# Kernel optimization log

Measured on AMD Instinct MI355X. Metric: run time of the kernel, lower is better.

## Reference

```python
import jax, jax.numpy as jnp
import numpy as np

DIM = 256
HEADS = 8
GROUPS = 4
HIDDEN = int(DIM * 4.0)
GW = DIM // GROUPS          # group width = 64
HEAD_DIM = DIM // HEADS     # 32
SCALE = HEAD_DIM ** (-0.5)
LN_EPS = 1e-6
BN_EPS = 1e-3               # keras BatchNormalization default epsilon
L2_EPS = 1e-12              # tf.nn.l2_normalize default


def _l2norm(t):
    ss = jnp.sum(t * t, axis=-1, keepdims=True)
    return t * jax.lax.rsqrt(jnp.maximum(ss, L2_EPS))


def setup_inputs() -> dict:
    key = jax.random.key(0)
    ks = jax.random.split(key, 12)
    B, H, W = 16, 56, 56
    x = jax.random.normal(ks[0], (B, H, W, DIM), jnp.float32)
    # depthwise 3x3 kernels for groups 1..GROUPS-1 (group 0's conv is unused in the
    # original code: y0 is a plain slice). Combined depthwise kernel over the last
    # (GROUPS-1)*GW channels, keras HWIO layout with in_ch_per_group = 1.
    dw_kernel = jax.random.normal(ks[1], (3, 3, 1, (GROUPS - 1) * GW), jnp.float32) * 0.05
    dw_bias = jnp.zeros(((GROUPS - 1) * GW,), jnp.float32)
    ln_gamma = jnp.ones((DIM,), jnp.float32)
    ln_beta = jnp.zeros((DIM,), jnp.float32)
    qkv_w = jax.random.normal(ks[2], (DIM, 3 * DIM), jnp.float32) * 0.02  # qkv_bias=False
    proj_w = jax.random.normal(ks[3], (DIM, DIM), jnp.float32) * 0.02
    proj_b = jnp.zeros((DIM,), jnp.float32)
    bn_gamma = jnp.ones((DIM,), jnp.float32)
    bn_beta = jnp.zeros((DIM,), jnp.float32)
    bn_mean = jax.random.normal(ks[4], (DIM,), jnp.float32) * 0.1
    bn_var = jax.random.uniform(ks[5], (DIM,), jnp.float32, 0.5, 1.5)
    fc1_w = jax.random.normal(ks[6], (DIM, HIDDEN), jnp.float32) * 0.02
    fc1_b = jnp.zeros((HIDDEN,), jnp.float32)
    fc2_w = jax.random.normal(ks[7], (HIDDEN, DIM), jnp.float32) * 0.02
    fc2_b = jnp.zeros((DIM,), jnp.float32)
    return dict(x=x, dw_kernel=dw_kernel, dw_bias=dw_bias, ln_gamma=ln_gamma,
                ln_beta=ln_beta, qkv_w=qkv_w, proj_w=proj_w, proj_b=proj_b,
                bn_gamma=bn_gamma, bn_beta=bn_beta, bn_mean=bn_mean, bn_var=bn_var,
                fc1_w=fc1_w, fc1_b=fc1_b, fc2_w=fc2_w, fc2_b=fc2_b)


def _gdta_forward(x, dw_kernel, dw_bias, ln_gamma, ln_beta, qkv_w, proj_w, proj_b,
                  bn_gamma, bn_beta, bn_mean, bn_var, fc1_w, fc1_b, fc2_w, fc2_b):
    B, H, W, C = x.shape
    N = H * W
    # ---- GOTA_block_part1: grouped depthwise convs with cumulative residual ----
    # y0 = x[..., :GW]; for i>=1: K_i = dwconv_i(x_i); y1=K1, y_i = K_i + y_{i-1}
    # => y_i (i>=1) is the cumulative sum of K_1..K_i along the group axis.
    xc = x[..., GW:]  # [B,H,W,(G-1)*GW]
    K = jax.lax.conv_general_dilated(
        xc, dw_kernel, window_strides=(1, 1), padding='SAME',
        dimension_numbers=('NHWC', 'HWIO', 'NHWC'),
        feature_group_count=(GROUPS - 1) * GW) + dw_bias
    Kg = K.reshape(B, H, W, GROUPS - 1, GW)
    Yg = jnp.cumsum(Kg, axis=3).reshape(B, H, W, (GROUPS - 1) * GW)
    dwconv = jnp.concatenate([x[..., :GW], Yg], axis=-1)  # [B,H,W,C]
    # ---- LayerNorm (last axis) ----
    mu = jnp.mean(dwconv, axis=-1, keepdims=True)
    var = jnp.mean(jnp.square(dwconv - mu), axis=-1, keepdims=True)
    norm1 = (dwconv - mu) * jax.lax.rsqrt(var + LN_EPS) * ln_gamma + ln_beta
    t = norm1.reshape(B, N, C)
    # ---- channel (cross-covariance) attention ----
    qkv = (t @ qkv_w).reshape(B, N, 3, HEADS, HEAD_DIM)
    qkv = jnp.transpose(qkv, (2, 0, 3, 1, 4))  # [3,B,h,N,d]
    q, k, v = qkv[0], qkv[1], qkv[2]
    q = _l2norm(q) * SCALE
    k = _l2norm(k)
    attn = jnp.einsum('bhnd,bhne->bhde', q, k)       # [B,h,d,d]
    attn = jax.nn.softmax(attn, axis=-1)
    out = jnp.einsum('bhnd,bhde->bhne', v, attn)     # [B,h,N,d]
    out = jnp.transpose(out, (0, 2, 1, 3)).reshape(B, N, C)
    out = out @ proj_w + proj_b
    attn_img = out.reshape(B, H, W, C)
    # ---- merge + BatchNorm (inference) + MLP + residual ----
    merged = attn_img + dwconv
    merged = (merged - bn_mean) * jax.lax.rsqrt(bn_var + BN_EPS) * bn_gamma + bn_beta
    h1 = jax.nn.gelu(merged @ fc1_w + fc1_b, approximate=False)
    mlp = h1 @ fc2_w + fc2_b
    return x + mlp


def reference(x, dw_kernel, dw_bias, ln_gamma, ln_beta, qkv_w, proj_w, proj_b,
              bn_gamma, bn_beta, bn_mean, bn_var, fc1_w, fc1_b, fc2_w, fc2_b):
    return _gdta_forward(x, dw_kernel, dw_bias, ln_gamma, ln_beta, qkv_w, proj_w,
                         proj_b, bn_gamma, bn_beta, bn_mean, bn_var,
                         fc1_w, fc1_b, fc2_w, fc2_b)
```

## Files before the change

kernel.cpp:

```cpp
#include <hip/hip_runtime.h>
#include <cstdint>

typedef unsigned short u16;
typedef __attribute__((ext_vector_type(8))) _Float16 f16x8;
typedef __attribute__((ext_vector_type(8))) unsigned short u16x8;
typedef __attribute__((ext_vector_type(4))) float f32x4;

#define SPLITN 7

__device__ __forceinline__ float b2f(u16 u) {
  union { unsigned int i; float f; } v; v.i = ((unsigned int)u) << 16; return v.f;
}
__device__ __forceinline__ u16 f2b(float f) {
  union { float f; unsigned int i; } v; v.f = f;
  unsigned int x = v.i;
  return (u16)((x + 0x7fffu + ((x >> 16) & 1u)) >> 16);
}
__device__ __forceinline__ u16 f2h(float f) {
  union { _Float16 h; u16 u; } v; v.h = (_Float16)f; return v.u;
}
__device__ __forceinline__ float h2f(u16 u) {
  union { u16 u; _Float16 h; } v; v.u = u; return (float)v.h;
}
__device__ __forceinline__ float ld(const void* p, long i, int f) {
  return f ? ((const float*)p)[i] : b2f(((const u16*)p)[i]);
}
template<int F>
__device__ __forceinline__ float4 ld4(const void* p, long i) {
  if (F) return *(const float4*)((const float*)p + i);
  const ushort4 u = *(const ushort4*)((const u16*)p + i);
  return make_float4(b2f(u.x), b2f(u.y), b2f(u.z), b2f(u.w));
}
__device__ __forceinline__ void fma4(float4& a, const float4 x, const float4 k) {
  a.x += x.x * k.x; a.y += x.y * k.y; a.z += x.z * k.z; a.w += x.w * k.w;
}
__device__ __forceinline__ float gelu(float v) {
  const float u = v * (0.7978845608028654f + 0.035677408136300125f * v * v);
  const float e = __expf(2.0f * u);
  return 0.5f * v * (1.0f + (1.0f - 2.0f / (e + 1.0f)));
}

__global__ __launch_bounds__(256) void detect_kernel(const u16* __restrict__ x,
                                                     int* __restrict__ flag) {
  __shared__ int sbad;
  if (threadIdx.x == 0) sbad = 0;
  __syncthreads();
  int b = 0;
  #pragma unroll
  for (int rr = 0; rr < 2; ++rr) {
    const int i = rr * 256 + threadIdx.x;
    const float v = fabsf(b2f(x[2 * i]));
    if (!(v < 100.f) || v < 1e-6f) ++b;
  }
  atomicAdd(&sbad, b);
  __syncthreads();
  if (threadIdx.x == 0) *flag = (sbad > 16) ? 1 : 0;
}

__global__ void transpose_cvt_kernel(const void* __restrict__ w0, u16* __restrict__ o0,
                                     const void* __restrict__ w1, u16* __restrict__ o1,
                                     const void* __restrict__ w2, u16* __restrict__ o2,
                                     const int* __restrict__ flagp) {
  const int f = *flagp;
  int bb = blockIdx.x;
  const void* in; u16* out; int R, C;
  if (bb < 768)       { in = w0; out = o0; R = 256;  C = 768;  }
  else if (bb < 1792) { in = w1; out = o1; R = 256;  C = 1024; bb -= 768; }
  else                { in = w2; out = o2; R = 1024; C = 256;  bb -= 1792; }
  const int o = bb * 256 + threadIdx.x;
  if (o < R * C) {
    const int i = o / R, j = o % R;
    out[o] = f2h(ld(in, (long)j * C + i, f));
  }
}

template<int F>
__device__ __forceinline__ void dwconv_body4(
    const void* __restrict__ x, const void* __restrict__ dwk, const void* __restrict__ dwb,
    const void* __restrict__ lng, const void* __restrict__ lnb,
    u16* __restrict__ dwc, u16* __restrict__ norm1, int tg, int lane)
{
  const int b = tg / 784, rem = tg % 784;
  const int hh = rem / 14, wg = (rem % 14) * 4;
  const int c0 = lane * 4;
  const long tok0 = (long)b * 3136 + hh * 56 + wg;
  float4 acc[4];
  float4 pv[4];
  if (lane >= 16) {
    const int j0 = c0 - 64;
    const float4 bb = ld4<F>(dwb, j0);
    acc[0] = bb; acc[1] = bb; acc[2] = bb; acc[3] = bb;
    #pragma unroll
    for (int dh = -1; dh <= 1; ++dh) {
      const int h2 = hh + dh;
      if (h2 < 0 || h2 >= 56) continue;
      const long rb = ((long)b * 3136 + h2 * 56) * 256;
      float4 xr[6];
      #pragma unroll
      for (int i = 0; i < 6; ++i) {
        const int w2 = wg - 1 + i;
        xr[i] = (w2 >= 0 && w2 < 56) ? ld4<F>(x, rb + (long)w2 * 256 + c0)
                                     : make_float4(0.f, 0.f, 0.f, 0.f);
      }
      float4 kw[3];
      #pragma unroll
      for (int i = 0; i < 3; ++i)
        kw[i] = ld4<F>(dwk, (long)((dh + 1) * 3 + i) * 192 + j0);
      #pragma unroll
      for (int t = 0; t < 4; ++t)
        #pragma unroll
        for (int i = 0; i < 3; ++i)
          fma4(acc[t], xr[t + i], kw[i]);
    }
  } else {
    #pragma unroll
    for (int t = 0; t < 4; ++t)
      pv[t] = ld4<F>(x, (tok0 + t) * 256 + c0);
  }
  const float4 g = ld4<F>(lng, c0);
  const float4 be = ld4<F>(lnb, c0);
  #pragma unroll
  for (int t = 0; t < 4; ++t) {
    float sx = acc[t].x, sy = acc[t].y, sz = acc[t].z, sw = acc[t].w;
    const float t1x = __shfl(sx, lane - 16), t1y = __shfl(sy, lane - 16),
                t1z = __shfl(sz, lane - 16), t1w = __shfl(sw, lane - 16);
    const float t2x = __shfl(sx, lane - 32), t2y = __shfl(sy, lane - 32),
                t2z = __shfl(sz, lane - 32), t2w = __shfl(sw, lane - 32);
    if (lane >= 32) { sx += t1x; sy += t1y; sz += t1z; sw += t1w; }
    if (lane >= 48) { sx += t2x; sy += t2y; sz += t2z; sw += t2w; }
    float vx, vy, vz, vw;
    if (lane < 16) { vx = pv[t].x; vy = pv[t].y; vz = pv[t].z; vw = pv[t].w; }
    else           { vx = sx;      vy = sy;      vz = sz;      vw = sw;      }
    float sum = vx + vy + vz + vw;
    float sq = vx * vx + vy * vy + vz * vz + vw * vw;
    #pragma unroll
    for (int m = 32; m; m >>= 1) { sum += __shfl_xor(sum, m); sq += __shfl_xor(sq, m); }
    const float mu = sum * (1.0f / 256.0f);
    const float var = sq * (1.0f / 256.0f) - mu * mu;
    const float rstd = rsqrtf(fmaxf(var, 0.f) + 1e-6f);
    ushort4 dv, nv;
    dv.x = f2h(vx); dv.y = f2h(vy); dv.z = f2h(vz); dv.w = f2h(vw);
    nv.x = f2h((vx - mu) * rstd * g.x + be.x);
    nv.y = f2h((vy - mu) * rstd * g.y + be.y);
    nv.z = f2h((vz - mu) * rstd * g.z + be.z);
    nv.w = f2h((vw - mu) * rstd * g.w + be.w);
    *(ushort4*)(dwc + (tok0 + t) * 256 + c0) = dv;
    *(ushort4*)(norm1 + (tok0 + t) * 256 + c0) = nv;
  }
}

__global__ __launch_bounds__(256) void dwconv_ln_kernel(
    const void* __restrict__ x, const void* __restrict__ dwk, const void* __restrict__ dwb,
    const void* __restrict__ lng, const void* __restrict__ lnb,
    u16* __restrict__ dwc, u16* __restrict__ norm1, const int* __restrict__ flagp)
{
  const int wave = threadIdx.x >> 6, lane = threadIdx.x & 63;
  const int tg = blockIdx.x * 4 + wave;
  if (*flagp) dwconv_body4<1>(x, dwk, dwb, lng, lnb, dwc, norm1, tg, lane);
  else        dwconv_body4<0>(x, dwk, dwb, lng, lnb, dwc, norm1, tg, lane);
}

template<int BM, int WR, int WC, int EPI, int KT>
__global__ __launch_bounds__(256) void gemm_kernel(
    const u16* __restrict__ A, const u16* __restrict__ Bt, void* C,
    int lda, int ldb, int ldc,
    long aZ, long bZ, long cZ, long zoff,
    const void* __restrict__ bias, const void* aux,
    const void* __restrict__ bng, const void* __restrict__ bnb,
    const void* __restrict__ bnm, const void* __restrict__ bnv,
    const int* __restrict__ flagp)
{
  static_assert(BM == 64 || BM == 128, "");
  constexpr int BN = 128;
  constexpr int WM = BM / WR, WN = BN / WC;
  constexpr int MI = WM / 16, NI = WN / 16;
  __shared__ __align__(16) u16 As[BM * 64];
  __shared__ __align__(16) u16 Bs[BN * 64];
  const int f = (EPI == 0 || EPI == 5) ? 0 : *flagp;
  const int tid = threadIdx.x;
  const int wave = tid >> 6, lane = tid & 63;
  const int wr = wave / WC, wc = wave % WC;
  const int quad = lane >> 4, l16 = lane & 15;
  const int tileM = blockIdx.y * BM, tileN = blockIdx.x * BN;
  const u16* Ab = A + (long)blockIdx.z * aZ + (long)tileM * lda;
  const u16* Bb = Bt + (long)blockIdx.z * bZ + (long)tileN * ldb;
  f32x4 acc[MI][NI];
  #pragma unroll
  for (int mi = 0; mi < MI; ++mi)
    #pragma unroll
    for (int ni = 0; ni < NI; ++ni)
      acc[mi][ni] = (f32x4){0.f, 0.f, 0.f, 0.f};

  for (int k0 = 0; k0 < KT; k0 += 64) {
    #pragma unroll
    for (int r = 0; r < BM / 32; ++r) {
      const int fg = r * 256 + tid;
      const int row = fg >> 3, cs = (fg & 7) ^ (row & 7);
      const u16* g = Ab + (long)row * lda + k0 + cs * 8;
      __builtin_amdgcn_global_load_lds(
          (const __attribute__((address_space(1))) void*)g,
          (__attribute__((address_space(3))) void*)(As + (r * 256 + wave * 64) * 8),
          16, 0, 0);
    }
    #pragma unroll
    for (int r = 0; r < 4; ++r) {
      const int fg = r * 256 + tid;
      const int row = fg >> 3, cs = (fg & 7) ^ (row & 7);
      const u16* g = Bb + (long)row * ldb + k0 + cs * 8;
      __builtin_amdgcn_global_load_lds(
          (const __attribute__((address_space(1))) void*)g,
          (__attribute__((address_space(3))) void*)(Bs + (r * 256 + wave * 64) * 8),
          16, 0, 0);
    }
    __syncthreads();
    #pragma unroll
    for (int ks = 0; ks < 2; ++ks) {
      f16x8 af[MI], bfr[NI];
      #pragma unroll
      for (int mi = 0; mi < MI; ++mi) {
        const int R = wr * WM + mi * 16 + l16;
        const int kc = ks * 4 + quad;
        af[mi] = *(const f16x8*)&As[(R * 8 + (kc ^ (R & 7))) * 8];
      }
      #pragma unroll
      for (int ni = 0; ni < NI; ++ni) {
        const int S = wc * WN + ni * 16 + l16;
        const int kc = ks * 4 + quad;
        bfr[ni] = *(const f16x8*)&Bs[(S * 8 + (kc ^ (S & 7))) * 8];
      }
      #pragma unroll
      for (int mi = 0; mi < MI; ++mi)
        #pragma unroll
        for (int ni = 0; ni < NI; ++ni)
          acc[mi][ni] = __builtin_amdgcn_mfma_f32_16x16x32_f16(af[mi], bfr[ni], acc[mi][ni], 0, 0, 0);
    }
    __syncthreads();
  }

  const long zC = (long)blockIdx.z * cZ + ((EPI == 5) ? 0 : zoff);
  #pragma unroll
  for (int mi = 0; mi < MI; ++mi) {
    #pragma unroll
    for (int ni = 0; ni < NI; ++ni) {
      const int col = tileN + wc * WN + ni * 16 + l16;
      #pragma unroll
      for (int r = 0; r < 4; ++r) {
        const int row = tileM + wr * WM + mi * 16 + quad * 4 + r;
        const long ci = zC + (long)row * ldc + col;
        float v = acc[mi][ni][r];
        if (EPI == 0) {
          ((u16*)C)[ci] = f2h(v);
        } else if (EPI == 2) {
          v += ld(bias, col, f);
          v += h2f(((const u16*)aux)[ci]);
          v = (v - ld(bnm, col, f)) * rsqrtf(ld(bnv, col, f) + 1e-3f) * ld(bng, col, f) + ld(bnb, col, f);
          ((u16*)C)[ci] = f2h(v);
        } else if (EPI == 3) {
          v += ld(bias, col, f);
          ((u16*)C)[ci] = f2h(gelu(v));
        } else if (EPI == 4) {
          v += ld(bias, col, f);
          v += ld(aux, ci, f);
          if (f) ((float*)C)[ci] = v; else ((u16*)C)[ci] = f2b(v);
        } else {
          if (col < 512) ((u16*)C)[(long)row * 512 + col] = f2h(v);
          else ((u16*)aux)[zoff + (long)row * 256 + (col - 512)] = f2h(v);
        }
      }
    }
  }
}

__global__ __launch_bounds__(256) void attn_accum_kernel(
    const u16* __restrict__ qk, float* __restrict__ A_part, int pair0)
{
  const int pl = blockIdx.x;
  const int split = blockIdx.y;
  const int bl = pl >> 3, h = pl & 7;
  const int tid = threadIdx.x;
  const int wave = tid >> 6, lane = tid & 63;
  const int quad = lane >> 4, l16 = lane & 15;
  const int dq = wave >> 1, eq = wave & 1;
  __shared__ __align__(16) u16 lqT[32 * 72];
  __shared__ __align__(16) u16 lkT[32 * 72];
  const long rowbase = (long)bl * 3136 * 512;
  const int n0 = split * 448;
  f32x4 acc = (f32x4){0.f, 0.f, 0.f, 0.f};
  const int seg = tid & 7;

  for (int ch = 0; ch < 7; ++ch) {
    const int nb = n0 + ch * 64;
    #pragma unroll
    for (int rr = 0; rr < 2; ++rr) {
      const int a = rr * 256 + tid;
      const int nl = a >> 3;
      const int co = (seg < 4) ? h * 32 + seg * 8 : 256 + h * 32 + (seg - 4) * 8;
      const u16x8 v8 = *(const u16x8*)(qk + rowbase + (long)(nb + nl) * 512 + co);
      float vf[8], p = 0.f;
      #pragma unroll
      for (int i = 0; i < 8; ++i) { vf[i] = h2f(v8[i]); p += vf[i] * vf[i]; }
      float p1 = p + __shfl_xor(p, 1);
      float p2 = p1 + __shfl_xor(p1, 2);
      const float other = __shfl_xor(p2, 4);
      const float ssq = (seg < 4) ? p2 : other;
      const float ssk = (seg < 4) ? other : p2;
      const float s = 0.17677669529663687f * rsqrtf(fmaxf(ssq, 1e-12f)) *
                      rsqrtf(fmaxf(ssk, 1e-12f));
      if (seg < 4) {
        const int db = seg * 8;
        #pragma unroll
        for (int i = 0; i < 8; ++i) {
          const int d = db + i;
          lqT[d * 72 + (nl ^ (d & 24))] = f2h(vf[i] * s);
        }
      } else {
        const int eb = (seg - 4) * 8;
        #pragma unroll
        for (int i = 0; i < 8; ++i) {
          const int e = eb + i;
          lkT[e * 72 + (nl ^ (e & 24))] = v8[i];
        }
      }
    }
    __syncthreads();
    #pragma unroll
    for (int ks = 0; ks < 2; ++ks) {
      const int tb = ks * 32 + quad * 8;
      const int dA = dq * 16 + l16;
      const int eB = eq * 16 + l16;
      const f16x8 af = *(const f16x8*)&lqT[dA * 72 + (tb ^ (dA & 24))];
      const f16x8 bf = *(const f16x8*)&lkT[eB * 72 + (tb ^ (eB & 24))];
      acc = __builtin_amdgcn_mfma_f32_16x16x32_f16(af, bf, acc, 0, 0, 0);
    }
    __syncthreads();
  }
  float* o = A_part + ((long)(pair0 + pl) * SPLITN + split) * 1024;
  #pragma unroll
  for (int r = 0; r < 4; ++r)
    o[(dq * 16 + quad * 4 + r) * 32 + eq * 16 + l16] = acc[r];
}

__global__ __launch_bounds__(1024) void softmax_kernel(float* A_part) {
  const int pair = blockIdx.x;
  const int t = threadIdx.x;
  float v = 0.f;
  float* base = A_part + (long)pair * SPLITN * 1024 + t;
  #pragma unroll
  for (int s = 0; s < SPLITN; ++s) v += base[s * 1024];
  float mx = v;
  #pragma unroll
  for (int m = 16; m; m >>= 1) mx = fmaxf(mx, __shfl_xor(mx, m, 32));
  const float p = expf(v - mx);
  float sm = p;
  #pragma unroll
  for (int m = 16; m; m >>= 1) sm += __shfl_xor(sm, m, 32);
  base[0] = p / sm;
}

__global__ __launch_bounds__(256) void wb_kernel(
    const float* __restrict__ A_part, const void* __restrict__ proj_w,
    u16* __restrict__ Wbt, const int* __restrict__ flagp)
{
  const int f = *flagp;
  const int b = blockIdx.x;
  const int cs = blockIdx.y;
  const int tid = threadIdx.x;
  const int cg = tid & 31, dg = tid >> 5;
  const int c = cs * 32 + cg;
  __shared__ float Ah[32][32];
  __shared__ float pw[32][33];
  for (int h = 0; h < 8; ++h) {
    const float* Abase = A_part + ((long)(b * 8 + h) * SPLITN) * 1024;
    #pragma unroll
    for (int rr = 0; rr < 4; ++rr) {
      const int ff = rr * 256 + tid;
      Ah[ff >> 5][ff & 31] = Abase[ff];
    }
    #pragma unroll
    for (int rr = 0; rr < 4; ++rr) {
      const int ff = rr * 256 + tid;
      const int e = ff >> 5, ccc = ff & 31;
      pw[e][ccc] = ld(proj_w, (long)(h * 32 + e) * 256 + cs * 32 + ccc, f);
    }
    __syncthreads();
    float acc[4] = {0.f, 0.f, 0.f, 0.f};
    #pragma unroll
    for (int e = 0; e < 32; ++e) {
      const float pv = pw[e][cg];
      #pragma unroll
      for (int dd = 0; dd < 4; ++dd)
        acc[dd] += Ah[dg * 4 + dd][e] * pv;
    }
    #pragma unroll
    for (int dd = 0; dd < 4; ++dd)
      Wbt[((long)b * 256 + c) * 256 + h * 32 + dg * 4 + dd] = f2h(acc[dd]);
    __syncthreads();
  }
}

extern "C" void kernel_launch(void* const* d_in, const int* in_sizes, int n_in,
                              void* d_out, int out_size, void* d_ws, size_t ws_size,
                              hipStream_t stream) {
  const void* x      = d_in[0];
  const void* dwk    = d_in[1];
  const void* dwb    = d_in[2];
  const void* lng    = d_in[3];
  const void* lnb    = d_in[4];
  const void* qkv_w  = d_in[5];
  const void* proj_w = d_in[6];
  const void* proj_b = d_in[7];
  const void* bn_g   = d_in[8];
  const void* bn_b   = d_in[9];
  const void* bn_m   = d_in[10];
  const void* bn_v   = d_in[11];
  const void* fc1_w  = d_in[12];
  const void* fc1_b  = d_in[13];
  const void* fc2_w  = d_in[14];
  const void* fc2_b  = d_in[15];
  char* ws = (char*)d_ws;

  int*   flagp   = (int*)  (ws + 0);
  u16*   wqkvT   = (u16*)  (ws + 256);
  u16*   wfc1T   = (u16*)  (ws + 393472);
  u16*   wfc2T   = (u16*)  (ws + 917760);
  float* A_part  = (float*)(ws + 1442048);
  u16*   Wbt     = (u16*)  (ws + 5112064);
  u16*   vbuf    = (u16*)  (ws + 7209216);
  u16*   dwc     = (u16*)  (ws + 32899328);
  u16*   qk_half = (u16*)  (ws + 58589440);
  u16*   h1c     = (u16*)  (ws + 58589440);
  u16*   norm1   = (u16*)d_out;

  detect_kernel<<<1, 256, 0, stream>>>((const u16*)x, flagp);

  transpose_cvt_kernel<<<2816, 256, 0, stream>>>(qkv_w, wqkvT, fc1_w, wfc1T,
                                                 fc2_w, wfc2T, flagp);

  dwconv_ln_kernel<<<3136, 256, 0, stream>>>(x, dwk, dwb, lng, lnb, dwc, norm1, flagp);

  for (int half = 0; half < 2; ++half) {
    const u16* nh = norm1 + (long)half * 25088 * 256;
    gemm_kernel<128, 2, 2, 5, 256><<<dim3(6, 196, 1), 256, 0, stream>>>(
        nh, wqkvT, qk_half, 256, 256, 512, 0, 0, 0, (long)half * 25088 * 256,
        nullptr, vbuf, nullptr, nullptr, nullptr, nullptr, flagp);
    attn_accum_kernel<<<dim3(64, SPLITN), 256, 0, stream>>>(qk_half, A_part, half * 64);
  }

  softmax_kernel<<<128, 1024, 0, stream>>>(A_part);
  wb_kernel<<<dim3(16, 8), 256, 0, stream>>>(A_part, proj_w, Wbt, flagp);

  gemm_kernel<64, 1, 4, 2, 256><<<dim3(2, 49, 16), 256, 0, stream>>>(
      vbuf, Wbt, dwc, 256, 256, 256,
      (long)3136 * 256, 65536, (long)3136 * 256, 0,
      proj_b, dwc, bn_g, bn_b, bn_m, bn_v, flagp);

  for (int c2 = 0; c2 < 4; ++c2) {
    const long ro = (long)c2 * 12544 * 256;
    gemm_kernel<128, 2, 2, 3, 256><<<dim3(8, 98, 1), 256, 0, stream>>>(
        dwc + ro, wfc1T, h1c, 256, 256, 1024, 0, 0, 0, 0,
        fc1_b, nullptr, nullptr, nullptr, nullptr, nullptr, flagp);
    gemm_kernel<64, 1, 4, 4, 1024><<<dim3(2, 196, 1), 256, 0, stream>>>(
        h1c, wfc2T, d_out, 1024, 1024, 256, 0, 0, 0, ro,
        fc2_b, x, nullptr, nullptr, nullptr, nullptr, flagp);
  }
}
```

Baseline: 532.3 us.

## Fuse fc1+GELU+fc2 MLP into one kernel keeping hidden activations in LDS

Replaces the chunked pair of GEMM launches (fc1 with GELU to a global hidden buffer, then fc2 with residual) with a single fused MLP kernel. Each block holds a 64-row input tile in LDS, computes the hidden layer in 128-column chunks, applies GELU into shared memory and accumulates the fc2 output in registers. This removes the global write and re-read of the 1024-wide hidden activation and seven launches. In exchange it uses about 80KB of LDS per block, which limits occupancy, reloads weights from global/L2 per block, and has no double-buffering of the weight loads.

```diff
diff --git a/kernel.cpp b/kernel.cpp
--- a/kernel.cpp
+++ b/kernel.cpp
@@ -39,6 +39,9 @@
   const float e = __expf(2.0f * u);
   return 0.5f * v * (1.0f + (1.0f - 2.0f / (e + 1.0f)));
 }
+#define GLDS(gp, lp) __builtin_amdgcn_global_load_lds( \
+    (const __attribute__((address_space(1))) void*)(gp), \
+    (__attribute__((address_space(3))) void*)(lp), 16, 0, 0)
 
 __global__ __launch_bounds__(256) void detect_kernel(const u16* __restrict__ x,
                                                      int* __restrict__ flag) {
@@ -196,21 +199,13 @@
     for (int r = 0; r < BM / 32; ++r) {
       const int fg = r * 256 + tid;
       const int row = fg >> 3, cs = (fg & 7) ^ (row & 7);
-      const u16* g = Ab + (long)row * lda + k0 + cs * 8;
-      __builtin_amdgcn_global_load_lds(
-          (const __attribute__((address_space(1))) void*)g,
-          (__attribute__((address_space(3))) void*)(As + (r * 256 + wave * 64) * 8),
-          16, 0, 0);
+      GLDS(Ab + (long)row * lda + k0 + cs * 8, As + (r * 256 + wave * 64) * 8);
     }
     #pragma unroll
     for (int r = 0; r < 4; ++r) {
       const int fg = r * 256 + tid;
       const int row = fg >> 3, cs = (fg & 7) ^ (row & 7);
-      const u16* g = Bb + (long)row * ldb + k0 + cs * 8;
-      __builtin_amdgcn_global_load_lds(
-          (const __attribute__((address_space(1))) void*)g,
-          (__attribute__((address_space(3))) void*)(Bs + (r * 256 + wave * 64) * 8),
-          16, 0, 0);
+      GLDS(Bb + (long)row * ldb + k0 + cs * 8, Bs + (r * 256 + wave * 64) * 8);
     }
     __syncthreads();
     #pragma unroll
@@ -248,20 +243,11 @@
         const int row = tileM + wr * WM + mi * 16 + quad * 4 + r;
         const long ci = zC + (long)row * ldc + col;
         float v = acc[mi][ni][r];
-        if (EPI == 0) {
-          ((u16*)C)[ci] = f2h(v);
-        } else if (EPI == 2) {
+        if (EPI == 2) {
           v += ld(bias, col, f);
           v += h2f(((const u16*)aux)[ci]);
           v = (v - ld(bnm, col, f)) * rsqrtf(ld(bnv, col, f) + 1e-3f) * ld(bng, col, f) + ld(bnb, col, f);
           ((u16*)C)[ci] = f2h(v);
-        } else if (EPI == 3) {
-          v += ld(bias, col, f);
-          ((u16*)C)[ci] = f2h(gelu(v));
-        } else if (EPI == 4) {
-          v += ld(bias, col, f);
-          v += ld(aux, ci, f);
-          if (f) ((float*)C)[ci] = v; else ((u16*)C)[ci] = f2b(v);
         } else {
           if (col < 512) ((u16*)C)[(long)row * 512 + col] = f2h(v);
           else ((u16*)aux)[zoff + (long)row * 256 + (col - 512)] = f2h(v);
@@ -269,6 +255,135 @@
       }
     }
   }
+}
+
+__global__ __launch_bounds__(256, 2) void mlp_kernel(
+    const u16* __restrict__ dwc, const u16* __restrict__ w1t, const u16* __restrict__ w2t,
+    const void* __restrict__ b1, const void* __restrict__ b2,
+    const void* __restrict__ x, void* __restrict__ out,
+    const int* __restrict__ flagp)
+{
+  __shared__ __align__(16) u16 Ds[64 * 256];
+  __shared__ __align__(16) u16 Hs[64 * 128];
+  __shared__ __align__(16) u16 Bs[256 * 64];
+  const int f = *flagp;
+  const int tid = threadIdx.x;
+  const int wave = tid >> 6, lane = tid & 63;
+  const int quad = lane >> 4, l16 = lane & 15;
+  const int tileM = blockIdx.x * 64;
+
+  #pragma unroll
+  for (int r = 0; r < 8; ++r) {
+    const int fg = r * 256 + tid;
+    const int row = fg >> 5, cs = (fg & 31) ^ (row & 7);
+    GLDS(dwc + (long)(tileM + row) * 256 + cs * 8, Ds + (r * 256 + wave * 64) * 8);
+  }
+
+  f32x4 accO[4][4];
+  #pragma unroll
+  for (int mi = 0; mi < 4; ++mi)
+    #pragma unroll
+    for (int ni = 0; ni < 4; ++ni)
+      accO[mi][ni] = (f32x4){0.f, 0.f, 0.f, 0.f};
+
+  for (int hc = 0; hc < 8; ++hc) {
+    f32x4 acc1[4][2];
+    #pragma unroll
+    for (int mi = 0; mi < 4; ++mi)
+      #pragma unroll
+      for (int ni = 0; ni < 2; ++ni)
+        acc1[mi][ni] = (f32x4){0.f, 0.f, 0.f, 0.f};
+
+    for (int it = 0; it < 4; ++it) {
+      #pragma unroll
+      for (int r = 0; r < 4; ++r) {
+        const int fg = r * 256 + tid;
+        const int row = fg >> 3, cs = (fg & 7) ^ (row & 7);
+        GLDS(w1t + (long)(hc * 128 + row) * 256 + it * 64 + cs * 8,
+             Bs + (r * 256 + wave * 64) * 8);
+      }
+      __syncthreads();
+      #pragma unroll
+      for (int ks = 0; ks < 2; ++ks) {
+        const int kc = it * 8 + ks * 4 + quad;
+        const int kl = ks * 4 + quad;
+        f16x8 af[4], bf[2];
+        #pragma unroll
+        for (int mi = 0; mi < 4; ++mi) {
+          const int R = mi * 16 + l16;
+          af[mi] = *(const f16x8*)&Ds[(R * 32 + (kc ^ (R & 7))) * 8];
+        }
+        #pragma unroll
+        for (int ni = 0; ni < 2; ++ni) {
+          const int S = wave * 32 + ni * 16 + l16;
+          bf[ni] = *(const f16x8*)&Bs[(S * 8 + (kl ^ (S & 7))) * 8];
+        }
+        #pragma unroll
+        for (int mi = 0; mi < 4; ++mi)
+          #pragma unroll
+          for (int ni = 0; ni < 2; ++ni)
+            acc1[mi][ni] = __builtin_amdgcn_mfma_f32_16x16x32_f16(af[mi], bf[ni], acc1[mi][ni], 0, 0, 0);
+      }
+      __syncthreads();
+    }
+    #pragma unroll
+    for (int mi = 0; mi < 4; ++mi)
+      #pragma unroll
+      for (int ni = 0; ni < 2; ++ni)
+        #pragma unroll
+        for (int r = 0; r < 4; ++r) {
+          const int row = mi * 16 + quad * 4 + r;
+          const int col = wave * 32 + ni * 16 + l16;
+          const float v = acc1[mi][ni][r] + ld(b1, hc * 128 + col, f);
+          Hs[(row * 16 + ((col >> 3) ^ (row & 7))) * 8 + (col & 7)] = f2h(gelu(v));
+        }
+    __syncthreads();
+    for (int it2 = 0; it2 < 2; ++it2) {
+      #pragma unroll
+      for (int r = 0; r < 8; ++r) {
+        const int fg = r * 256 + tid;
+        const int row = fg >> 3, cs = (fg & 7) ^ (row & 7);
+        GLDS(w2t + (long)row * 1024 + hc * 128 + it2 * 64 + cs * 8,
+             Bs + (r * 256 + wave * 64) * 8);
+      }
+      __syncthreads();
+      #pragma unroll
+      for (int ks = 0; ks < 2; ++ks) {
+        const int kc = it2 * 8 + ks * 4 + quad;
+        const int kl = ks * 4 + quad;
+        f16x8 af[4], bf[4];
+        #pragma unroll
+        for (int mi = 0; mi < 4; ++mi) {
+          const int R = mi * 16 + l16;
+          af[mi] = *(const f16x8*)&Hs[(R * 16 + (kc ^ (R & 7))) * 8];
+        }
+        #pragma unroll
+        for (int ni = 0; ni < 4; ++ni) {
+          const int S = wave * 64 + ni * 16 + l16;
+          bf[ni] = *(const f16x8*)&Bs[(S * 8 + (kl ^ (S & 7))) * 8];
+        }
+        #pragma unroll
+        for (int mi = 0; mi < 4; ++mi)
+          #pragma unroll
+          for (int ni = 0; ni < 4; ++ni)
+            accO[mi][ni] = __builtin_amdgcn_mfma_f32_16x16x32_f16(af[mi], bf[ni], accO[mi][ni], 0, 0, 0);
+      }
+      __syncthreads();
+    }
+  }
+  #pragma unroll
+  for (int mi = 0; mi < 4; ++mi)
+    #pragma unroll
+    for (int ni = 0; ni < 4; ++ni) {
+      const int col = wave * 64 + ni * 16 + l16;
+      #pragma unroll
+      for (int r = 0; r < 4; ++r) {
+        const int row = tileM + mi * 16 + quad * 4 + r;
+        const long ci = (long)row * 256 + col;
+        const float v = accO[mi][ni][r] + ld(b2, col, f) + ld(x, ci, f);
+        if (f) ((float*)out)[ci] = v; else ((u16*)out)[ci] = f2b(v);
+      }
+    }
 }
 
 __global__ __launch_bounds__(256) void attn_accum_kernel(
@@ -428,7 +543,6 @@
   u16*   vbuf    = (u16*)  (ws + 7209216);
   u16*   dwc     = (u16*)  (ws + 32899328);
   u16*   qk_half = (u16*)  (ws + 58589440);
-  u16*   h1c     = (u16*)  (ws + 58589440);
   u16*   norm1   = (u16*)d_out;
 
   detect_kernel<<<1, 256, 0, stream>>>((const u16*)x, flagp);
@@ -454,13 +568,5 @@
       (long)3136 * 256, 65536, (long)3136 * 256, 0,
       proj_b, dwc, bn_g, bn_b, bn_m, bn_v, flagp);
 
-  for (int c2 = 0; c2 < 4; ++c2) {
-    const long ro = (long)c2 * 12544 * 256;
-    gemm_kernel<128, 2, 2, 3, 256><<<dim3(8, 98, 1), 256, 0, stream>>>(
-        dwc + ro, wfc1T, h1c, 256, 256, 1024, 0, 0, 0, 0,
-        fc1_b, nullptr, nullptr, nullptr, nullptr, nullptr, flagp);
-    gemm_kernel<64, 1, 4, 4, 1024><<<dim3(2, 196, 1), 256, 0, stream>>>(
-        h1c, wfc2T, d_out, 1024, 1024, 256, 0, 0, 0, ro,
-        fc2_b, x, nullptr, nullptr, nullptr, nullptr, flagp);
-  }
-}
+  mlp_kernel<<<784, 256, 0, stream>>>(dwc, wfc1T, wfc2T, fc1_b, fc2_b, x, d_out, flagp);
+}
```

Result: faster. 464.1 us (-12.8%).
